# Kernel tuning notes

Measured on AMD Instinct MI355X. Metric: run time of the kernel, lower is better.

The kernel has to match this reference:

```python
import jax, jax.numpy as jnp
import numpy as np

B, C, H = 4, 1, 256          # batch, channels, square image size
A, P = 180, 256              # n_angles, n_detector_positions
T = int(np.ceil(np.sqrt(2.0) * H))  # samples per ray (covers image diagonal) = 363


def setup_inputs() -> dict:
    key = jax.random.key(0)
    x = jax.random.normal(key, (B, C, H, H), dtype=jnp.float32)
    # projection angles uniformly covering [0, pi)
    thetas = (jnp.pi * jnp.arange(A, dtype=jnp.float32) / A)
    # detector offsets in pixel units, centered on the image center
    positions = jnp.arange(P, dtype=jnp.float32) - (P - 1) / 2.0
    return {"x": x, "thetas": thetas, "positions": positions}


def _radon(x, thetas, positions):
    """Radon transform: line integrals along rays (theta, s) with bilinear
    sampling at unit spacing along each ray. Returns sinogram [B,C,A,P]."""
    Bc, Cc, Hh, Ww = x.shape
    cx = (Ww - 1) / 2.0
    cy = (Hh - 1) / 2.0
    t = jnp.arange(T, dtype=x.dtype) - (T - 1) / 2.0          # [T] along-ray param
    cos = jnp.cos(thetas)[:, None, None]                       # [A,1,1]
    sin = jnp.sin(thetas)[:, None, None]
    s = positions[None, :, None]                               # [1,P,1]
    tt = t[None, None, :]                                      # [1,1,T]
    # rotated ray sample coordinates, [A,P,T]
    px = cx + s * cos - tt * sin
    py = cy + s * sin + tt * cos
    x0 = jnp.floor(px)
    y0 = jnp.floor(py)
    wx = px - x0
    wy = py - y0
    x0i = x0.astype(jnp.int32)
    y0i = y0.astype(jnp.int32)

    def gather(iy, ix):
        # zero outside the image (zero-padding boundary)
        valid = (ix >= 0) & (ix < Ww) & (iy >= 0) & (iy < Hh)
        ixc = jnp.clip(ix, 0, Ww - 1)
        iyc = jnp.clip(iy, 0, Hh - 1)
        v = x[:, :, iyc, ixc]                                  # [B,C,A,P,T]
        return v * valid.astype(x.dtype)

    interp = (gather(y0i,     x0i)     * ((1.0 - wx) * (1.0 - wy))
            + gather(y0i,     x0i + 1) * (wx * (1.0 - wy))
            + gather(y0i + 1, x0i)     * ((1.0 - wx) * wy)
            + gather(y0i + 1, x0i + 1) * (wx * wy))
    return interp.sum(axis=-1)                                 # [B,C,A,P]


def reference(x, thetas, positions):
    return _radon(x, thetas, positions)
```

## Files before the change

### kernel.cpp

```cpp
#include <hip/hip_runtime.h>
#include <hip/hip_fp16.h>

#define NB   4
#define NA   180
#define NP   256
#define NH   256
#define NW   256
#define NT   363
#define GANG 3
#define NSEG 4
#define TSEG 91

#define ROWS 259
#define COLS 262
#define IMG_HALFS (ROWS * COLS)
#define IMG_DWORDS (IMG_HALFS / 2)
#define IMG_BYTES (IMG_HALFS * 2)
#define RED_BYTES (NP * NSEG * 4)
#define SMEM_BYTES (IMG_BYTES + RED_BYTES)

extern "C" __global__ __launch_bounds__(1024)
void radon_fwd(const float* __restrict__ x,
               const float* __restrict__ thetas,
               const float* __restrict__ positions,
               float* __restrict__ out)
{
    extern __shared__ unsigned char smem[];
    __half2*      img2  = (__half2*)smem;
    unsigned int* imgw  = (unsigned int*)smem;
    float*        red   = (float*)(smem + IMG_BYTES);

    const int tid = threadIdx.x + (threadIdx.y << 8);
    const int b   = blockIdx.y;
    const float* __restrict__ xb = x + b * (NH * NW);

    for (int i = tid; i < IMG_DWORDS; i += 1024) imgw[i] = 0u;
    __syncthreads();

    const float2* src2 = (const float2*)xb;
    for (int j = tid; j < (NH * NW) / 2; j += 1024) {
        float2 v = src2[j];
        int r = j >> 7;
        int k = j & 127;
        img2[(r + 1) * 131 + k + 1] =
            __halves2half2(__float2half_rn(v.x), __float2half_rn(v.y));
    }
    __syncthreads();

    const int   p   = threadIdx.x;
    const int   seg = threadIdx.y;
    const float s   = positions[p];
    const int   a0  = blockIdx.x * GANG;
    const int   t0  = seg * TSEG;

    float accs[GANG];
    for (int g = 0; g < GANG; ++g) {
        const float th  = thetas[a0 + g];
        const float cv  = cosf(th);
        const float sv  = sinf(th);
        const float nsv = -sv;
        const float bx2 = fmaf(s, cv, 129.5f);
        const float by1 = fmaf(s, sv, 128.5f);
        float acc = 0.f;
        #pragma unroll 4
        for (int t = 0; t < TSEG; ++t) {
            const float ftv = (float)(t0 + t) - 181.0f;
            float px = fmaf(ftv, nsv, bx2);
            float py = fmaf(ftv, cv,  by1);
            px = __builtin_amdgcn_fmed3f(px, 1.0f, 258.0f);
            py = __builtin_amdgcn_fmed3f(py, 0.0f, 257.0f);
            const float fx = floorf(px);
            const float fy = floorf(py);
            const float wx = px - fx;
            const float wy = py - fy;
            const int a  = (int)fmaf(fy, 262.0f, fx);
            const int k  = a >> 1;
            const unsigned int sh = (a & 1) << 4;
            const unsigned int d0 = imgw[k];
            const unsigned int d1 = imgw[k + 1];
            const unsigned int d2 = imgw[k + 131];
            const unsigned int d3 = imgw[k + 132];
            unsigned int p0 =
                (unsigned int)(((((unsigned long long)d1) << 32) | d0) >> sh);
            unsigned int p1 =
                (unsigned int)(((((unsigned long long)d3) << 32) | d2) >> sh);
            const float2 f0 = __half22float2(*reinterpret_cast<__half2*>(&p0));
            const float2 f1 = __half22float2(*reinterpret_cast<__half2*>(&p1));
            const float h0 = fmaf(wx, f0.y - f0.x, f0.x);
            const float h1 = fmaf(wx, f1.y - f1.x, f1.x);
            acc = fmaf(wy, h1 - h0, acc + h0);
        }
        accs[g] = acc;
    }

    for (int g = 0; g < GANG; ++g) {
        __syncthreads();
        red[(seg << 8) + p] = accs[g];
        __syncthreads();
        if (seg == 0) {
            float r4 = red[p] + red[256 + p] + red[512 + p] + red[768 + p];
            out[b * (NA * NP) + (a0 + g) * NP + p] = r4;
        }
    }
}

extern "C" void kernel_launch(void* const* d_in, const int* in_sizes, int n_in,
                              void* d_out, int out_size, void* d_ws, size_t ws_size,
                              hipStream_t stream) {
    const float* x         = (const float*)d_in[0];
    const float* thetas    = (const float*)d_in[1];
    const float* positions = (const float*)d_in[2];
    float* out = (float*)d_out;

    hipFuncSetAttribute((const void*)radon_fwd,
                        hipFuncAttributeMaxDynamicSharedMemorySize, SMEM_BYTES);

    dim3 grid(NA / GANG, NB);
    dim3 block(NP, NSEG);
    radon_fwd<<<grid, block, SMEM_BYTES, stream>>>(x, thetas, positions, out);
}
```

Measured before the change: 125.6 us.

## Split image into halves per block to halve LDS footprint and double occupancy

Each block now stages only half the image (a row half for near-vertical angles, a column half otherwise) into LDS, so the LDS footprint roughly halves and two blocks can share a CU. The launch grid doubles along z. Each ray's sample range is cut at the half boundary, and partial sums are combined with atomicAdd into an output that is zeroed by a memset first. The along-ray samples are now interleaved across segments, and the vertical interpolation step uses packed half2 FMA. The cost is an extra memset, atomics, reduced fp16 precision in the interpolation, and fragile boundary handling at the split.

```diff
diff --git a/kernel.cpp b/kernel.cpp
--- a/kernel.cpp
+++ b/kernel.cpp
@@ -1,23 +1,57 @@
 #include <hip/hip_runtime.h>
 #include <hip/hip_fp16.h>
+
 
 #define NB   4
 #define NA   180
 #define NP   256
-#define NH   256
-#define NW   256
-#define NT   363
 #define GANG 3
 #define NSEG 4
-#define TSEG 91
 
-#define ROWS 259
-#define COLS 262
-#define IMG_HALFS (ROWS * COLS)
-#define IMG_DWORDS (IMG_HALFS / 2)
-#define IMG_BYTES (IMG_HALFS * 2)
-#define RED_BYTES (NP * NSEG * 4)
-#define SMEM_BYTES (IMG_BYTES + RED_BYTES)
+#define IMG_DW_MAX 17353
+#define RED_OFF ((IMG_DW_MAX + 1) * 4)
+#define SMEM_BYTES (RED_OFF + NP * NSEG * 4)
+
+template<int STRIDE_DW>
+__device__ __forceinline__ float ray_accum(
+    const unsigned int* __restrict__ imgw,
+    float bxr, float byr, float nsv, float cv,
+    float xlo, float xhi, float ylo, float yhi,
+    int tlo, int thi, int seg)
+{
+    float acc = 0.f;
+    int   t  = tlo + seg;
+    float tf = (float)t - 181.0f;
+    #pragma unroll 4
+    for (; t < thi; t += 4, tf += 4.0f) {
+        float px = fmaf(tf, nsv, bxr);
+        float py = fmaf(tf, cv,  byr);
+        px = __builtin_amdgcn_fmed3f(px, xlo, xhi);
+        py = __builtin_amdgcn_fmed3f(py, ylo, yhi);
+        const float fx = floorf(px);
+        const float fy = floorf(py);
+        const float wx = px - fx;
+        const float wy = py - fy;
+        const int a = (int)fmaf(fy, (float)(2 * STRIDE_DW), fx);
+        const int kd = a >> 1;
+        const unsigned sh = (a & 1) << 4;
+        const unsigned d0 = imgw[kd];
+        const unsigned d1 = imgw[kd + 1];
+        const unsigned d2 = imgw[kd + STRIDE_DW];
+        const unsigned d3 = imgw[kd + STRIDE_DW + 1];
+        unsigned q0 = (unsigned)(((((unsigned long long)d1) << 32) | d0) >> sh);
+        unsigned q1 = (unsigned)(((((unsigned long long)d3) << 32) | d2) >> sh);
+        const __half2 h0 = *reinterpret_cast<__half2*>(&q0);
+        const __half2 h1 = *reinterpret_cast<__half2*>(&q1);
+        const __half2 dv  = __hsub2(h1, h0);
+        const __half2 wy2 = __half2half2(__float2half_rn(wy));
+        const __half2 V   = __hfma2(wy2, dv, h0);
+        const float vlo = __half2float(__low2half(V));
+        const float vhi = __half2float(__high2half(V));
+        acc = fmaf(wx, vhi - vlo, acc + vlo);
+    }
+    return acc;
+}
 
 extern "C" __global__ __launch_bounds__(1024)
 void radon_fwd(const float* __restrict__ x,
@@ -26,32 +60,60 @@
                float* __restrict__ out)
 {
     extern __shared__ unsigned char smem[];
-    __half2*      img2  = (__half2*)smem;
-    unsigned int* imgw  = (unsigned int*)smem;
-    float*        red   = (float*)(smem + IMG_BYTES);
+    unsigned int* imgw = (unsigned int*)smem;
+    __half2*      img2 = (__half2*)smem;
+    float*        red  = (float*)(smem + RED_OFF);
 
+    const int grp  = blockIdx.x;
+    const int b    = blockIdx.y;
+    const int half = blockIdx.z;
+    const int a0   = grp * GANG;
+    const bool regA = (a0 < 45) || (a0 >= 135);
     const int tid = threadIdx.x + (threadIdx.y << 8);
-    const int b   = blockIdx.y;
-    const float* __restrict__ xb = x + b * (NH * NW);
+    const float* __restrict__ xb = x + b * 65536;
 
-    for (int i = tid; i < IMG_DWORDS; i += 1024) imgw[i] = 0u;
+    for (int i = tid; i <= IMG_DW_MAX; i += 1024) imgw[i] = 0u;
     __syncthreads();
 
-    const float2* src2 = (const float2*)xb;
-    for (int j = tid; j < (NH * NW) / 2; j += 1024) {
-        float2 v = src2[j];
-        int r = j >> 7;
-        int k = j & 127;
-        img2[(r + 1) * 131 + k + 1] =
-            __halves2half2(__float2half_rn(v.x), __float2half_rn(v.y));
+    if (regA) {
+        const int rbase  = half ? 126 : 0;
+        const int rowoff = half ? 0 : 1;
+        const float2* src2 = (const float2*)(xb + rbase * 256);
+        for (int j = tid; j < 130 * 128; j += 1024) {
+            const int rr = j >> 7;
+            const int k  = j & 127;
+            float2 v = src2[rr * 128 + k];
+            img2[(rr + rowoff) * 131 + k + 1] = __floats2half2_rn(v.x, v.y);
+        }
+    } else {
+        const int cbase2 = half ? 62 : 0;
+        const int coff   = half ? 0 : 1;
+        const float2* src2 = (const float2*)xb;
+        for (int rr = tid >> 6; rr < 256; rr += 16) {
+            for (int c2 = tid & 63; c2 < 66; c2 += 64) {
+                float2 v = src2[rr * 128 + cbase2 + c2];
+                img2[(rr + 1) * 67 + c2 + coff] = __floats2half2_rn(v.x, v.y);
+            }
+        }
     }
     __syncthreads();
+
+    float xlo, xhi, ylo, yhi;
+    if (regA) {
+        xlo = 1.f; xhi = 258.f;
+        if (half == 0) { ylo = 0.f; yhi = 129.984375f; }
+        else           { ylo = 1.f; yhi = 130.f; }
+    } else {
+        ylo = 0.f; yhi = 257.f;
+        if (half == 0) { xlo = 1.f; xhi = 130.984375f; }
+        else           { xlo = 3.f; xhi = 132.f; }
+    }
+    const float rebY = (regA && half) ? 127.f : 0.f;
+    const float rebX = (!regA && half) ? 126.f : 0.f;
 
     const int   p   = threadIdx.x;
     const int   seg = threadIdx.y;
     const float s   = positions[p];
-    const int   a0  = blockIdx.x * GANG;
-    const int   t0  = seg * TSEG;
 
     float accs[GANG];
     for (int g = 0; g < GANG; ++g) {
@@ -61,36 +123,21 @@
         const float nsv = -sv;
         const float bx2 = fmaf(s, cv, 129.5f);
         const float by1 = fmaf(s, sv, 128.5f);
-        float acc = 0.f;
-        #pragma unroll 4
-        for (int t = 0; t < TSEG; ++t) {
-            const float ftv = (float)(t0 + t) - 181.0f;
-            float px = fmaf(ftv, nsv, bx2);
-            float py = fmaf(ftv, cv,  by1);
-            px = __builtin_amdgcn_fmed3f(px, 1.0f, 258.0f);
-            py = __builtin_amdgcn_fmed3f(py, 0.0f, 257.0f);
-            const float fx = floorf(px);
-            const float fy = floorf(py);
-            const float wx = px - fx;
-            const float wy = py - fy;
-            const int a  = (int)fmaf(fy, 262.0f, fx);
-            const int k  = a >> 1;
-            const unsigned int sh = (a & 1) << 4;
-            const unsigned int d0 = imgw[k];
-            const unsigned int d1 = imgw[k + 1];
-            const unsigned int d2 = imgw[k + 131];
-            const unsigned int d3 = imgw[k + 132];
-            unsigned int p0 =
-                (unsigned int)(((((unsigned long long)d1) << 32) | d0) >> sh);
-            unsigned int p1 =
-                (unsigned int)(((((unsigned long long)d3) << 32) | d2) >> sh);
-            const float2 f0 = __half22float2(*reinterpret_cast<__half2*>(&p0));
-            const float2 f1 = __half22float2(*reinterpret_cast<__half2*>(&p1));
-            const float h0 = fmaf(wx, f0.y - f0.x, f0.x);
-            const float h1 = fmaf(wx, f1.y - f1.x, f1.x);
-            acc = fmaf(wy, h1 - h0, acc + h0);
-        }
-        accs[g] = acc;
+        const float slope = regA ? cv : nsv;
+        const float base  = regA ? by1 : bx2;
+        const float thr   = regA ? 129.f : 130.f;
+        const float tstar = 181.0f + (thr - base) / slope;
+        const float Sf    = (slope > 0.f) ? ceilf(tstar) : (floorf(tstar) + 1.0f);
+        const int   S     = (int)fmaxf(0.f, fminf(364.f, Sf));
+        const bool  h0Low = (slope > 0.f);
+        int lo, hi;
+        if ((half == 0) == h0Low) { lo = 0; hi = S; }
+        else                      { lo = S; hi = 364; }
+        const float bxr = bx2 - rebX;
+        const float byr = by1 - rebY;
+        accs[g] = regA
+            ? ray_accum<131>(imgw, bxr, byr, nsv, cv, xlo, xhi, ylo, yhi, lo, hi, seg)
+            : ray_accum< 67>(imgw, bxr, byr, nsv, cv, xlo, xhi, ylo, yhi, lo, hi, seg);
     }
 
     for (int g = 0; g < GANG; ++g) {
@@ -99,7 +146,7 @@
         __syncthreads();
         if (seg == 0) {
             float r4 = red[p] + red[256 + p] + red[512 + p] + red[768 + p];
-            out[b * (NA * NP) + (a0 + g) * NP + p] = r4;
+            atomicAdd(&out[b * (NA * NP) + (a0 + g) * NP + p], r4);
         }
     }
 }
@@ -115,7 +162,9 @@
     hipFuncSetAttribute((const void*)radon_fwd,
                         hipFuncAttributeMaxDynamicSharedMemorySize, SMEM_BYTES);
 
-    dim3 grid(NA / GANG, NB);
+    hipMemsetAsync(d_out, 0, (size_t)out_size * sizeof(float), stream);
+
+    dim3 grid(NA / GANG, NB, 2);
     dim3 block(NP, NSEG);
     radon_fwd<<<grid, block, SMEM_BYTES, stream>>>(x, thetas, positions, out);
 }
```

Measured after the change: 128.1 us. About the same (+2.0%).
